# Kernel tuning notes

Measured on AMD Instinct MI355X. Metric: run time of the kernel, lower is better.

The kernel has to match this reference:

```python
import jax, jax.numpy as jnp
import numpy as np

N_HEADS = 32
N_KV = 8
HEAD_DIM = 128
ROPE_THETA = 10000.0
PAST_LEN = 2048


def _rope_cos_sin(position_ids):
    # inv_freq: [head_dim/2]
    inv_freq = 1.0 / (ROPE_THETA ** (jnp.arange(0, HEAD_DIM, 2, dtype=jnp.float32) / HEAD_DIM))
    freqs = position_ids.astype(jnp.float32)[..., None] * inv_freq  # [B, S, hd/2]
    emb = jnp.concatenate([freqs, freqs], axis=-1)  # [B, S, hd]
    return jnp.cos(emb), jnp.sin(emb)


def _rotate_half(x):
    x1, x2 = jnp.split(x, 2, axis=-1)
    return jnp.concatenate([-x2, x1], axis=-1)


def setup_inputs() -> dict:
    key = jax.random.key(0)
    ks = jax.random.split(key, 10)
    B, S = 1, 2048
    IN = 8192
    s = 0.02
    return {
        "hidden_states": jax.random.normal(ks[0], (B, S, IN), jnp.float32),
        "position_ids": (jnp.arange(S, dtype=jnp.int32) + PAST_LEN)[None, :],
        "cache_k": jax.random.normal(ks[1], (B, N_KV, PAST_LEN, HEAD_DIM), jnp.float32),
        "cache_v": jax.random.normal(ks[2], (B, N_KV, PAST_LEN, HEAD_DIM), jnp.float32),
        "Wq": jax.random.normal(ks[3], (N_HEADS * HEAD_DIM, IN), jnp.float32) * s,
        "bq": jax.random.normal(ks[4], (N_HEADS * HEAD_DIM,), jnp.float32) * s,
        "Wk": jax.random.normal(ks[5], (N_KV * HEAD_DIM, IN), jnp.float32) * s,
        "bk": jax.random.normal(ks[6], (N_KV * HEAD_DIM,), jnp.float32) * s,
        "Wv": jax.random.normal(ks[7], (N_KV * HEAD_DIM, IN), jnp.float32) * s,
        "bv": jax.random.normal(ks[8], (N_KV * HEAD_DIM,), jnp.float32) * s,
        "Wo": jax.random.normal(ks[9], (N_HEADS * HEAD_DIM, N_HEADS * HEAD_DIM), jnp.float32) * s,
    }


def reference(hidden_states, position_ids, cache_k, cache_v, Wq, bq, Wk, bk, Wv, bv, Wo):
    B, Sq, _ = hidden_states.shape
    G = N_HEADS // N_KV

    # QKV projections -> [B, H, S, D]
    q = (hidden_states @ Wq.T + bq).reshape(B, Sq, N_HEADS, HEAD_DIM).transpose(0, 2, 1, 3)
    k = (hidden_states @ Wk.T + bk).reshape(B, Sq, N_KV, HEAD_DIM).transpose(0, 2, 1, 3)
    v = (hidden_states @ Wv.T + bv).reshape(B, Sq, N_KV, HEAD_DIM).transpose(0, 2, 1, 3)

    # RoPE
    cos, sin = _rope_cos_sin(position_ids)  # [B, Sq, D]
    cos, sin = cos[:, None], sin[:, None]   # broadcast over heads
    q = q * cos + _rotate_half(q) * sin
    k = k * cos + _rotate_half(k) * sin

    # KV cache concat
    key = jnp.concatenate([cache_k, k], axis=2)   # [B, Kv, Sk, D]
    value = jnp.concatenate([cache_v, v], axis=2)
    Sk = key.shape[2]
    past_len = Sk - Sq

    # GQA attention (grouped einsum == repeat_interleave + SDPA)
    qg = q.reshape(B, N_KV, G, Sq, HEAD_DIM)
    scale = 1.0 / jnp.sqrt(jnp.float32(HEAD_DIM))
    scores = jnp.einsum("bkgqd,bkld->bkgql", qg, key) * scale  # [B, Kv, G, Sq, Sk]

    q_pos = past_len + jnp.arange(Sq)
    mask = jnp.arange(Sk)[None, :] <= q_pos[:, None]  # [Sq, Sk]
    scores = jnp.where(mask[None, None, None], scores, -jnp.inf)
    attn = jax.nn.softmax(scores, axis=-1)

    ctx = jnp.einsum("bkgql,bkld->bkgqd", attn, value)
    ctx = ctx.reshape(B, N_HEADS, Sq, HEAD_DIM).transpose(0, 2, 1, 3).reshape(B, Sq, N_HEADS * HEAD_DIM)
    out = ctx @ Wo.T
    return out, key, value
```

## Files before the change

### kernel.cpp

```cpp
#include <hip/hip_runtime.h>
#include <hip/hip_bf16.h>
#include <math.h>

typedef float f32x4 __attribute__((ext_vector_type(4)));
typedef short s16x8 __attribute__((ext_vector_type(8)));
typedef __bf16 bf16x8 __attribute__((ext_vector_type(8)));

__device__ __forceinline__ unsigned short f2bf(float f) {
  return __builtin_bit_cast(unsigned short, (__bf16)f);
}

__device__ __forceinline__ f32x4 mfma16(s16x8 a, s16x8 b, f32x4 c) {
  return __builtin_amdgcn_mfma_f32_16x16x32_bf16(
      __builtin_bit_cast(bf16x8, a), __builtin_bit_cast(bf16x8, b), c, 0, 0, 0);
}

#define GLDS(gp, lp) __builtin_amdgcn_global_load_lds(                      \
    (__attribute__((address_space(1))) void*)(gp),                          \
    (__attribute__((address_space(3))) void*)(lp), 16, 0, 0)

struct __attribute__((aligned(8))) us4 { unsigned short x, y, z, w; };
__device__ __forceinline__ us4 cvt4(float4 v) {
  us4 r; r.x = f2bf(v.x); r.y = f2bf(v.y); r.z = f2bf(v.z); r.w = f2bf(v.w);
  return r;
}

__global__ __launch_bounds__(256) void conv_all(
    const float4* __restrict__ h, const float4* __restrict__ wq,
    const float4* __restrict__ wk, const float4* __restrict__ wv,
    const float4* __restrict__ wo, const float4* __restrict__ bq,
    const float4* __restrict__ bk, const float4* __restrict__ bv,
    us4* __restrict__ hbf, us4* __restrict__ wqkvbf, us4* __restrict__ wobf,
    float4* __restrict__ biasc)
{
  const unsigned int U = 20973056u;
  const unsigned int stride = gridDim.x * blockDim.x;
  for (unsigned int u = blockIdx.x * blockDim.x + threadIdx.x; u < U; u += stride) {
    if (u < 4194304u) {
      hbf[u] = cvt4(h[u]);
    } else if (u < 12582912u) {
      unsigned int o = u - 4194304u;  wqkvbf[o] = cvt4(wq[o]);
    } else if (u < 14680064u) {
      unsigned int o = u - 12582912u; wqkvbf[8388608u + o] = cvt4(wk[o]);
    } else if (u < 16777216u) {
      unsigned int o = u - 14680064u; wqkvbf[10485760u + o] = cvt4(wv[o]);
    } else if (u < 20971520u) {
      unsigned int o = u - 16777216u; wobf[o] = cvt4(wo[o]);
    } else {
      unsigned int o = u - 20971520u;
      float4 v = (o < 1024u) ? bq[o] : (o < 1280u) ? bk[o - 1024u] : bv[o - 1280u];
      biasc[o] = v;
    }
  }
}

__global__ __launch_bounds__(256) void rope_table(const int* __restrict__ pos_ids,
                                                  float* __restrict__ cost,
                                                  float* __restrict__ sint)
{
  int idx = blockIdx.x * blockDim.x + threadIdx.x;
  if (idx >= 131072) return;
  int s = idx >> 6, i = idx & 63;
  double invf = exp(-((double)i / 64.0) * 9.210340371976184);
  double ang = (double)pos_ids[s] * invf;
  cost[idx] = (float)cos(ang);
  sint[idx] = (float)sin(ang);
}

template<int NF>
__global__ __launch_bounds__(512, 2) void gemm8p(const unsigned short* __restrict__ A,
                                                 const unsigned short* __restrict__ B,
                                                 const float* __restrict__ bias,
                                                 float* __restrict__ C,
                                                 int M, int N, int K)
{
  constexpr int BN = NF * 64;
  constexpr int BUFSZ = 32768 + BN * 128;
  __shared__ char smem[2 * BUFSZ];
  const int tid = threadIdx.x;
  const int l = tid & 63;
  const int w = tid >> 6;
  const int wm = w >> 2, wn = w & 3;
  const int wr = wm * 128;
  const int wc = wn * (16 * NF);
  const int lk16 = (l >> 4) * 16;

  const int nwg = gridDim.x;
  const int s = (blockIdx.x & 7) * (nwg >> 3) + (blockIdx.x >> 3);
  const int NBY = M >> 8;
  const int by = s % NBY, bx = s / NBY;
  const size_t arow0 = (size_t)by * 256;
  const size_t brow0 = (size_t)bx * BN;
  const size_t Kb = (size_t)K * 2;
  const char* Ab = (const char*)A;
  const char* Bb = (const char*)B;

  f32x4 acc[8][NF];
#pragma unroll
  for (int i = 0; i < 8; ++i)
#pragma unroll
    for (int j = 0; j < NF; ++j) acc[i][j] = (f32x4){0.f, 0.f, 0.f, 0.f};

  auto STAGE = [&](int t, char* buf) {
    const size_t k0b = (size_t)t * 128;
#pragma unroll
    for (int cc = 0; cc < 4; ++cc) {
      const int ch = cc * 512 + tid;
      const int r = ch >> 3;
      const int c2s = ((ch & 7) * 16) ^ ((r & 7) << 4);
      GLDS(Ab + (arow0 + r) * Kb + k0b + c2s, buf + ch * 16);
    }
#pragma unroll
    for (int cc = 0; cc < NF; ++cc) {
      const int ch = cc * 512 + tid;
      const int r = ch >> 3;
      const int c2s = ((ch & 7) * 16) ^ ((r & 7) << 4);
      GLDS(Bb + (brow0 + r) * Kb + k0b + c2s, buf + 32768 + ch * 16);
    }
  };

  const int nt = K >> 6;
  STAGE(0, smem);
  asm volatile("s_waitcnt vmcnt(0)" ::: "memory");
  __builtin_amdgcn_s_barrier();

  for (int t = 0; t < nt; ++t) {
    char* cur = smem + (t & 1) * BUFSZ;
    if (t + 1 < nt) STAGE(t + 1, smem + ((t + 1) & 1) * BUFSZ);
    s16x8 bfr[NF][2];
#pragma unroll
    for (int qd = 0; qd < 4; ++qd) {
      s16x8 afr[2][2];
#pragma unroll
      for (int i = 0; i < 2; ++i)
#pragma unroll
        for (int k = 0; k < 2; ++k) {
          const int r = wr + (qd * 2 + i) * 16 + (l & 15);
          const int c2 = k * 64 + lk16;
          afr[i][k] = *(const s16x8*)(cur + (r * 128 + (c2 ^ ((r & 7) << 4))));
        }
      if (qd == 0) {
#pragma unroll
        for (int n = 0; n < NF; ++n)
#pragma unroll
          for (int k = 0; k < 2; ++k) {
            const int r = wc + n * 16 + (l & 15);
            const int c2 = k * 64 + lk16;
            bfr[n][k] = *(const s16x8*)(cur + 32768 + (r * 128 + (c2 ^ ((r & 7) << 4))));
          }
      }
      asm volatile("" ::: "memory");
      __builtin_amdgcn_s_barrier();
      __builtin_amdgcn_s_setprio(1);
#pragma unroll
      for (int i = 0; i < 2; ++i)
#pragma unroll
        for (int n = 0; n < NF; ++n)
#pragma unroll
          for (int k = 0; k < 2; ++k)
            acc[qd * 2 + i][n] = mfma16(afr[i][k], bfr[n][k], acc[qd * 2 + i][n]);
      __builtin_amdgcn_s_setprio(0);
      asm volatile("" ::: "memory");
      __builtin_amdgcn_s_barrier();
    }
    asm volatile("s_waitcnt vmcnt(0)" ::: "memory");
    __builtin_amdgcn_s_barrier();
  }

  const int r0 = (int)arow0 + wr + (l >> 4) * 4;
  const int c0 = (int)brow0 + wc + (l & 15);
#pragma unroll
  for (int mi = 0; mi < 8; ++mi) {
#pragma unroll
    for (int ni = 0; ni < NF; ++ni) {
      const int c = c0 + ni * 16;
      const float bvv = bias ? bias[c] : 0.f;
#pragma unroll
      for (int rr = 0; rr < 4; ++rr) {
        const int r = r0 + mi * 16 + rr;
        C[(size_t)r * N + c] = acc[mi][ni][rr] + bvv;
      }
    }
  }
}

__global__ __launch_bounds__(256) void rope_scatter(
    const float* __restrict__ qkv, const float* __restrict__ cost,
    const float* __restrict__ sint, const float* __restrict__ cache_k,
    const float* __restrict__ cache_v, float* __restrict__ keyout,
    float* __restrict__ valout, unsigned short* __restrict__ qbf,
    char* __restrict__ kswz, char* __restrict__ vswz)
{
  const float rs = 0.08838834764831845f;
  const int stride = gridDim.x * blockDim.x;
  for (int idx = blockIdx.x * blockDim.x + threadIdx.x; idx < 11534336; idx += stride) {
    if (idx < 4194304) {
      int i = idx & 63, hh = (idx >> 6) & 31, s = idx >> 11;
      const float* base = qkv + (size_t)s * 6144 + hh * 128 + i;
      float q1 = base[0], q2 = base[64];
      float c = cost[s * 64 + i], sn = sint[s * 64 + i];
      float o1 = (q1 * c - q2 * sn) * rs, o2 = (q2 * c + q1 * sn) * rs;
      unsigned short* qd = qbf + ((size_t)hh * 2048 + s) * 128 + i;
      qd[0] = f2bf(o1); qd[64] = f2bf(o2);
    } else if (idx < 5242880) {
      int j = idx - 4194304;
      int i = j & 63, kh = (j >> 6) & 7, s = j >> 9;
      const float* base = qkv + (size_t)s * 6144 + 4096 + kh * 128 + i;
      float k1 = base[0], k2 = base[64];
      float c = cost[s * 64 + i], sn = sint[s * 64 + i];
      float o1 = k1 * c - k2 * sn, o2 = k2 * c + k1 * sn;
      float* kd = keyout + ((size_t)kh * 4096 + 2048 + s) * 128 + i;
      kd[0] = o1; kd[64] = o2;
      int t = 32 + (s >> 6), r = s & 63;
      char* tb = kswz + (size_t)(kh * 64 + t) * 16384;
      *(unsigned short*)(tb + ((r * 256 + i * 2) ^ ((r & 7) << 4))) = f2bf(o1);
      *(unsigned short*)(tb + ((r * 256 + (i + 64) * 2) ^ ((r & 7) << 4))) = f2bf(o2);
    } else if (idx < 7340032) {
      int j = idx - 5242880;
      int d = j & 127, kh = (j >> 7) & 7, s = j >> 10;
      float v = qkv[(size_t)s * 6144 + 5120 + kh * 128 + d];
      valout[((size_t)kh * 4096 + 2048 + s) * 128 + d] = v;
      int t = 32 + (s >> 6), c = s & 63;
      char* tb = vswz + (size_t)(kh * 64 + t) * 16384;
      *(unsigned short*)(tb + ((d * 128 + c * 2) ^ ((d & 7) << 4))) = f2bf(v);
    } else if (idx < 9437184) {
      int j = idx - 7340032;
      int d = j & 127, s = (j >> 7) & 2047, kh = j >> 18;
      float v = cache_k[(size_t)(kh * 2048 + s) * 128 + d];
      keyout[((size_t)kh * 4096 + s) * 128 + d] = v;
      int t = s >> 6, r = s & 63;
      char* tb = kswz + (size_t)(kh * 64 + t) * 16384;
      *(unsigned short*)(tb + ((r * 256 + d * 2) ^ ((r & 7) << 4))) = f2bf(v);
    } else {
      int j = idx - 9437184;
      int d = j & 127, s = (j >> 7) & 2047, kh = j >> 18;
      float v = cache_v[(size_t)(kh * 2048 + s) * 128 + d];
      valout[((size_t)kh * 4096 + s) * 128 + d] = v;
      int t = s >> 6, c = s & 63;
      char* tb = vswz + (size_t)(kh * 64 + t) * 16384;
      *(unsigned short*)(tb + ((d * 128 + c * 2) ^ ((d & 7) << 4))) = f2bf(v);
    }
  }
}

__global__ __launch_bounds__(512) void attn_fwd(const unsigned short* __restrict__ qbf,
                                                const char* __restrict__ kswz,
                                                const char* __restrict__ vswz,
                                                unsigned short* __restrict__ ctx)
{
  __shared__ char smem[81920];
  char* Ps = smem + 65536;
  const int tid = threadIdx.x;
  const int l = tid & 63;
  const int w = tid >> 6;
  const int d = blockIdx.x;
  const int b = d >> 5;
  const int qt = (b < 8) ? b : 23 - b;
  const int h = (d & 7) * 4 + ((d >> 3) & 3);
  const int kh = h >> 2;
  const int nt = 2 * qt + 34;
  const int qrow16 = (l >> 4) * 4;
  const float L2E = 1.44269504f;

  s16x8 aq[4];
  {
    const int qr = qt * 128 + w * 16 + (l & 15);
    const unsigned short* qp = qbf + ((size_t)h * 2048 + qr) * 128 + (l >> 4) * 8;
#pragma unroll
    for (int kc = 0; kc < 4; ++kc) aq[kc] = *(const s16x8*)(qp + kc * 32);
  }
  f32x4 o[8];
#pragma unroll
  for (int i = 0; i < 8; ++i) o[i] = (f32x4){0.f, 0.f, 0.f, 0.f};
  float m[4]  = {-1e30f, -1e30f, -1e30f, -1e30f};
  float m2[4] = {-1e30f, -1e30f, -1e30f, -1e30f};
  float ls[4] = {0.f, 0.f, 0.f, 0.f};

  const char* kb0 = kswz + (size_t)kh * (64 * 16384);
  const char* vb0 = vswz + (size_t)kh * (64 * 16384);
  char* Pw = Ps + w * 2048;

  auto STAGE = [&](int t, int c) {
    const char* kb = kb0 + (size_t)t * 16384;
    const char* vb = vb0 + (size_t)t * 16384;
    char* Kt = smem + c * 32768;
    char* Vt = Kt + 16384;
#pragma unroll
    for (int j = 0; j < 2; ++j) {
      const int cw = j * 8 + w;
      GLDS(kb + (cw * 64 + l) * 16, Kt + cw * 1024);
      GLDS(vb + (cw * 64 + l) * 16, Vt + cw * 1024);
    }
  };

  STAGE(0, 0);
  int c = 0;
  for (int t = 0; t < nt; ++t) {
    asm volatile("s_waitcnt vmcnt(0)" ::: "memory");
    __builtin_amdgcn_s_barrier();
    asm volatile("" ::: "memory");
    if (t + 1 < nt) STAGE(t + 1, c ^ 1);
    const char* Kt = smem + c * 32768;
    const char* Vt = Kt + 16384;

    f32x4 s[4];
#pragma unroll
    for (int i = 0; i < 4; ++i) s[i] = (f32x4){0.f, 0.f, 0.f, 0.f};
    __builtin_amdgcn_s_setprio(1);
#pragma unroll
    for (int kc = 0; kc < 4; ++kc) {
      const int d0b = (kc * 32 + (l >> 4) * 8) * 2;
#pragma unroll
      for (int ni = 0; ni < 4; ++ni) {
        const int row = ni * 16 + (l & 15);
        s16x8 kf = *(const s16x8*)(Kt + ((row * 256 + d0b) ^ ((row & 7) << 4)));
        s[ni] = mfma16(aq[kc], kf, s[ni]);
      }
    }
    __builtin_amdgcn_s_setprio(0);
    if (t >= nt - 2) {
      const int qpos_b = 2048 + qt * 128 + w * 16 + qrow16;
      const int kvcol = (l & 15);
#pragma unroll
      for (int ni = 0; ni < 4; ++ni) {
        const int kvpos = t * 64 + ni * 16 + kvcol;
#pragma unroll
        for (int rr = 0; rr < 4; ++rr)
          if (kvpos > qpos_b + rr) s[ni][rr] = -1e30f;
      }
    }
    float rm[4];
#pragma unroll
    for (int rr = 0; rr < 4; ++rr)
      rm[rr] = fmaxf(fmaxf(s[0][rr], s[1][rr]), fmaxf(s[2][rr], s[3][rr]));
#pragma unroll
    for (int rr = 0; rr < 4; ++rr) {
      float v = rm[rr];
      v = fmaxf(v, __shfl_xor(v, 1));
      v = fmaxf(v, __shfl_xor(v, 2));
      v = fmaxf(v, __shfl_xor(v, 4));
      v = fmaxf(v, __shfl_xor(v, 8));
      rm[rr] = v;
    }
    const bool ok = (rm[0] <= m[0] + 8.f) && (rm[1] <= m[1] + 8.f) &&
                    (rm[2] <= m[2] + 8.f) && (rm[3] <= m[3] + 8.f);
    if (!__all(ok)) {
      float fs[4];
#pragma unroll
      for (int rr = 0; rr < 4; ++rr) {
        const float nm = fmaxf(m[rr], rm[rr]);
        fs[rr] = __builtin_amdgcn_exp2f((m[rr] - nm) * L2E);
        m[rr] = nm;
        m2[rr] = nm * L2E;
      }
#pragma unroll
      for (int i = 0; i < 8; ++i)
#pragma unroll
        for (int rr = 0; rr < 4; ++rr) o[i][rr] *= fs[rr];
#pragma unroll
      for (int rr = 0; rr < 4; ++rr) ls[rr] *= fs[rr];
    }
#pragma unroll
    for (int ni = 0; ni < 4; ++ni) {
      const int colb = (ni * 16 + (l & 15)) * 2;
#pragma unroll
      for (int rr = 0; rr < 4; ++rr) {
        const float p = __builtin_amdgcn_exp2f(__builtin_fmaf(s[ni][rr], L2E, -m2[rr]));
        ls[rr] += p;
        const int q = qrow16 + rr;
        *(__bf16*)(Pw + ((q * 128 + colb) ^ ((q & 7) << 4))) = (__bf16)p;
      }
    }
    s16x8 pa[2];
#pragma unroll
    for (int kc2 = 0; kc2 < 2; ++kc2) {
      const int q = l & 15;
      const int kvb = (kc2 * 32 + (l >> 4) * 8) * 2;
      pa[kc2] = *(const s16x8*)(Pw + ((q * 128 + kvb) ^ ((q & 7) << 4)));
    }
    __builtin_amdgcn_s_setprio(1);
#pragma unroll
    for (int sub = 0; sub < 8; ++sub) {
      const int dd = sub * 16 + (l & 15);
#pragma unroll
      for (int kc2 = 0; kc2 < 2; ++kc2) {
        const int kvb = (kc2 * 32 + (l >> 4) * 8) * 2;
        s16x8 vf = *(const s16x8*)(Vt + ((dd * 128 + kvb) ^ ((dd & 7) << 4)));
        o[sub] = mfma16(pa[kc2], vf, o[sub]);
      }
    }
    __builtin_amdgcn_s_setprio(0);
    asm volatile("" ::: "memory");
    c ^= 1;
  }

#pragma unroll
  for (int rr = 0; rr < 4; ++rr) {
    float v = ls[rr];
    v += __shfl_xor(v, 1);
    v += __shfl_xor(v, 2);
    v += __shfl_xor(v, 4);
    v += __shfl_xor(v, 8);
    ls[rr] = 1.0f / v;
  }
  const int r0 = qt * 128 + w * 16 + qrow16;
  const int c0 = h * 128 + (l & 15);
#pragma unroll
  for (int sub = 0; sub < 8; ++sub)
#pragma unroll
    for (int rr = 0; rr < 4; ++rr) {
      const float v = o[sub][rr] * ls[rr];
      ctx[(size_t)(r0 + rr) * 4096 + c0 + sub * 16] = f2bf(v);
    }
}

extern "C" void kernel_launch(void* const* d_in, const int* in_sizes, int n_in,
                              void* d_out, int out_size, void* d_ws, size_t ws_size,
                              hipStream_t stream) {
  (void)in_sizes; (void)n_in; (void)out_size; (void)ws_size;
  const float* hs     = (const float*)d_in[0];
  const int*   pos    = (const int*)d_in[1];
  const float* cachek = (const float*)d_in[2];
  const float* cachev = (const float*)d_in[3];
  const float* Wq     = (const float*)d_in[4];
  const float* bq     = (const float*)d_in[5];
  const float* Wk     = (const float*)d_in[6];
  const float* bk     = (const float*)d_in[7];
  const float* Wv     = (const float*)d_in[8];
  const float* bv     = (const float*)d_in[9];
  const float* Wo     = (const float*)d_in[10];

  float* out    = (float*)d_out;
  float* keyout = out + (size_t)2048 * 4096;
  float* valout = keyout + (size_t)8 * 4096 * 128;

  char* ws = (char*)d_ws;
  unsigned short* hbf    = (unsigned short*)(ws + 0);
  unsigned short* qbf    = (unsigned short*)(ws + 0);
  char*           kswz   = ws + 16777216;
  char*           vswz   = ws + 25165824;
  unsigned short* wqkvbf = (unsigned short*)(ws + 33554432);
  unsigned short* wobf   = (unsigned short*)(ws + 134217728);
  float*          qkvf   = (float*)(ws + 167772160);
  unsigned short* ctxbf  = (unsigned short*)(ws + 167772160);
  float*          cost   = (float*)(ws + 218103808);
  float*          sint   = (float*)(ws + 218628096);
  float*          biasc  = (float*)(ws + 219152384);

  conv_all<<<2048, 256, 0, stream>>>((const float4*)hs, (const float4*)Wq,
                                     (const float4*)Wk, (const float4*)Wv,
                                     (const float4*)Wo, (const float4*)bq,
                                     (const float4*)bk, (const float4*)bv,
                                     (us4*)hbf, (us4*)wqkvbf, (us4*)wobf,
                                     (float4*)biasc);
  rope_table<<<512, 256, 0, stream>>>(pos, cost, sint);
  gemm8p<3><<<256, 512, 0, stream>>>(hbf, wqkvbf, biasc, qkvf, 2048, 6144, 8192);
  rope_scatter<<<2048, 256, 0, stream>>>(qkvf, cost, sint, cachek, cachev,
                                         keyout, valout, qbf, kswz, vswz);
  attn_fwd<<<512, 512, 0, stream>>>(qbf, kswz, vswz, ctxbf);
  gemm8p<2><<<256, 512, 0, stream>>>(ctxbf, wobf, nullptr, out, 2048, 4096, 4096);
}
```

Measured before the change: 637.0 us.

## Process two 16-row query tiles per wave in attention kernel

Attention block now uses 4 waves of 256 threads instead of 8, and each wave handles 32 query rows as two 16-row sub-tiles. Each K and V fragment read from LDS feeds two MFMAs, halving LDS read traffic per unit of compute. The cost is roughly doubled accumulator and score registers per wave, which may lower occupancy or cause spills, and fewer waves are left to hide latency.

```diff
diff --git a/kernel.cpp b/kernel.cpp
--- a/kernel.cpp
+++ b/kernel.cpp
@@ -243,7 +243,7 @@
   }
 }
 
-__global__ __launch_bounds__(512) void attn_fwd(const unsigned short* __restrict__ qbf,
+__global__ __launch_bounds__(256) void attn_fwd(const unsigned short* __restrict__ qbf,
                                                 const char* __restrict__ kswz,
                                                 const char* __restrict__ vswz,
                                                 unsigned short* __restrict__ ctx)
@@ -253,32 +253,38 @@
   const int tid = threadIdx.x;
   const int l = tid & 63;
   const int w = tid >> 6;
+  const int g = l >> 4;
   const int d = blockIdx.x;
   const int b = d >> 5;
   const int qt = (b < 8) ? b : 23 - b;
   const int h = (d & 7) * 4 + ((d >> 3) & 3);
   const int kh = h >> 2;
   const int nt = 2 * qt + 34;
-  const int qrow16 = (l >> 4) * 4;
+  const int qrow16 = g * 4;
   const float L2E = 1.44269504f;
 
-  s16x8 aq[4];
-  {
-    const int qr = qt * 128 + w * 16 + (l & 15);
-    const unsigned short* qp = qbf + ((size_t)h * 2048 + qr) * 128 + (l >> 4) * 8;
-#pragma unroll
-    for (int kc = 0; kc < 4; ++kc) aq[kc] = *(const s16x8*)(qp + kc * 32);
-  }
-  f32x4 o[8];
-#pragma unroll
-  for (int i = 0; i < 8; ++i) o[i] = (f32x4){0.f, 0.f, 0.f, 0.f};
-  float m[4]  = {-1e30f, -1e30f, -1e30f, -1e30f};
-  float m2[4] = {-1e30f, -1e30f, -1e30f, -1e30f};
-  float ls[4] = {0.f, 0.f, 0.f, 0.f};
+  s16x8 aq[2][4];
+#pragma unroll
+  for (int qs = 0; qs < 2; ++qs) {
+    const int qr = qt * 128 + w * 32 + qs * 16 + (l & 15);
+    const unsigned short* qp = qbf + ((size_t)h * 2048 + qr) * 128 + g * 8;
+#pragma unroll
+    for (int kc = 0; kc < 4; ++kc) aq[qs][kc] = *(const s16x8*)(qp + kc * 32);
+  }
+  f32x4 o[2][8];
+#pragma unroll
+  for (int qs = 0; qs < 2; ++qs)
+#pragma unroll
+    for (int i = 0; i < 8; ++i) o[qs][i] = (f32x4){0.f, 0.f, 0.f, 0.f};
+  float m[2][4], m2[2][4], ls[2][4];
+#pragma unroll
+  for (int qs = 0; qs < 2; ++qs)
+#pragma unroll
+    for (int rr = 0; rr < 4; ++rr) { m[qs][rr] = -1e30f; m2[qs][rr] = -1e30f; ls[qs][rr] = 0.f; }
 
   const char* kb0 = kswz + (size_t)kh * (64 * 16384);
   const char* vb0 = vswz + (size_t)kh * (64 * 16384);
-  char* Pw = Ps + w * 2048;
+  char* Pw = Ps + w * 4096;
 
   auto STAGE = [&](int t, int c) {
     const char* kb = kb0 + (size_t)t * 16384;
@@ -286,8 +292,8 @@
     char* Kt = smem + c * 32768;
     char* Vt = Kt + 16384;
 #pragma unroll
-    for (int j = 0; j < 2; ++j) {
-      const int cw = j * 8 + w;
+    for (int j = 0; j < 4; ++j) {
+      const int cw = j * 4 + w;
       GLDS(kb + (cw * 64 + l) * 16, Kt + cw * 1024);
       GLDS(vb + (cw * 64 + l) * 16, Vt + cw * 1024);
     }
@@ -303,90 +309,108 @@
     const char* Kt = smem + c * 32768;
     const char* Vt = Kt + 16384;
 
-    f32x4 s[4];
-#pragma unroll
-    for (int i = 0; i < 4; ++i) s[i] = (f32x4){0.f, 0.f, 0.f, 0.f};
+    f32x4 s[2][4];
+#pragma unroll
+    for (int qs = 0; qs < 2; ++qs)
+#pragma unroll
+      for (int i = 0; i < 4; ++i) s[qs][i] = (f32x4){0.f, 0.f, 0.f, 0.f};
     __builtin_amdgcn_s_setprio(1);
 #pragma unroll
     for (int kc = 0; kc < 4; ++kc) {
-      const int d0b = (kc * 32 + (l >> 4) * 8) * 2;
+      const int d0b = (kc * 32 + g * 8) * 2;
 #pragma unroll
       for (int ni = 0; ni < 4; ++ni) {
         const int row = ni * 16 + (l & 15);
         s16x8 kf = *(const s16x8*)(Kt + ((row * 256 + d0b) ^ ((row & 7) << 4)));
-        s[ni] = mfma16(aq[kc], kf, s[ni]);
+        s[0][ni] = mfma16(aq[0][kc], kf, s[0][ni]);
+        s[1][ni] = mfma16(aq[1][kc], kf, s[1][ni]);
       }
     }
     __builtin_amdgcn_s_setprio(0);
     if (t >= nt - 2) {
-      const int qpos_b = 2048 + qt * 128 + w * 16 + qrow16;
       const int kvcol = (l & 15);
 #pragma unroll
+      for (int qs = 0; qs < 2; ++qs) {
+        const int qpos_b = 2048 + qt * 128 + w * 32 + qs * 16 + qrow16;
+#pragma unroll
+        for (int ni = 0; ni < 4; ++ni) {
+          const int kvpos = t * 64 + ni * 16 + kvcol;
+#pragma unroll
+          for (int rr = 0; rr < 4; ++rr)
+            if (kvpos > qpos_b + rr) s[qs][ni][rr] = -1e30f;
+        }
+      }
+    }
+    float rm[2][4];
+#pragma unroll
+    for (int qs = 0; qs < 2; ++qs)
+#pragma unroll
+      for (int rr = 0; rr < 4; ++rr) {
+        float v = fmaxf(fmaxf(s[qs][0][rr], s[qs][1][rr]),
+                        fmaxf(s[qs][2][rr], s[qs][3][rr]));
+        v = fmaxf(v, __shfl_xor(v, 1));
+        v = fmaxf(v, __shfl_xor(v, 2));
+        v = fmaxf(v, __shfl_xor(v, 4));
+        v = fmaxf(v, __shfl_xor(v, 8));
+        rm[qs][rr] = v;
+      }
+    bool ok = true;
+#pragma unroll
+    for (int qs = 0; qs < 2; ++qs)
+#pragma unroll
+      for (int rr = 0; rr < 4; ++rr) ok = ok && (rm[qs][rr] <= m[qs][rr] + 8.f);
+    if (!__all(ok)) {
+#pragma unroll
+      for (int qs = 0; qs < 2; ++qs) {
+        float fs[4];
+#pragma unroll
+        for (int rr = 0; rr < 4; ++rr) {
+          const float nm = fmaxf(m[qs][rr], rm[qs][rr]);
+          fs[rr] = __builtin_amdgcn_exp2f((m[qs][rr] - nm) * L2E);
+          m[qs][rr] = nm;
+          m2[qs][rr] = nm * L2E;
+        }
+#pragma unroll
+        for (int i = 0; i < 8; ++i)
+#pragma unroll
+          for (int rr = 0; rr < 4; ++rr) o[qs][i][rr] *= fs[rr];
+#pragma unroll
+        for (int rr = 0; rr < 4; ++rr) ls[qs][rr] *= fs[rr];
+      }
+    }
+#pragma unroll
+    for (int qs = 0; qs < 2; ++qs)
+#pragma unroll
       for (int ni = 0; ni < 4; ++ni) {
-        const int kvpos = t * 64 + ni * 16 + kvcol;
-#pragma unroll
-        for (int rr = 0; rr < 4; ++rr)
-          if (kvpos > qpos_b + rr) s[ni][rr] = -1e30f;
-      }
-    }
-    float rm[4];
-#pragma unroll
-    for (int rr = 0; rr < 4; ++rr)
-      rm[rr] = fmaxf(fmaxf(s[0][rr], s[1][rr]), fmaxf(s[2][rr], s[3][rr]));
-#pragma unroll
-    for (int rr = 0; rr < 4; ++rr) {
-      float v = rm[rr];
-      v = fmaxf(v, __shfl_xor(v, 1));
-      v = fmaxf(v, __shfl_xor(v, 2));
-      v = fmaxf(v, __shfl_xor(v, 4));
-      v = fmaxf(v, __shfl_xor(v, 8));
-      rm[rr] = v;
-    }
-    const bool ok = (rm[0] <= m[0] + 8.f) && (rm[1] <= m[1] + 8.f) &&
-                    (rm[2] <= m[2] + 8.f) && (rm[3] <= m[3] + 8.f);
-    if (!__all(ok)) {
-      float fs[4];
-#pragma unroll
-      for (int rr = 0; rr < 4; ++rr) {
-        const float nm = fmaxf(m[rr], rm[rr]);
-        fs[rr] = __builtin_amdgcn_exp2f((m[rr] - nm) * L2E);
-        m[rr] = nm;
-        m2[rr] = nm * L2E;
-      }
-#pragma unroll
-      for (int i = 0; i < 8; ++i)
-#pragma unroll
-        for (int rr = 0; rr < 4; ++rr) o[i][rr] *= fs[rr];
-#pragma unroll
-      for (int rr = 0; rr < 4; ++rr) ls[rr] *= fs[rr];
-    }
-#pragma unroll
-    for (int ni = 0; ni < 4; ++ni) {
-      const int colb = (ni * 16 + (l & 15)) * 2;
-#pragma unroll
-      for (int rr = 0; rr < 4; ++rr) {
-        const float p = __builtin_amdgcn_exp2f(__builtin_fmaf(s[ni][rr], L2E, -m2[rr]));
-        ls[rr] += p;
-        const int q = qrow16 + rr;
-        *(__bf16*)(Pw + ((q * 128 + colb) ^ ((q & 7) << 4))) = (__bf16)p;
-      }
-    }
-    s16x8 pa[2];
-#pragma unroll
-    for (int kc2 = 0; kc2 < 2; ++kc2) {
-      const int q = l & 15;
-      const int kvb = (kc2 * 32 + (l >> 4) * 8) * 2;
-      pa[kc2] = *(const s16x8*)(Pw + ((q * 128 + kvb) ^ ((q & 7) << 4)));
-    }
+        const int colb = (ni * 16 + (l & 15)) * 2;
+#pragma unroll
+        for (int rr = 0; rr < 4; ++rr) {
+          const float p =
+              __builtin_amdgcn_exp2f(__builtin_fmaf(s[qs][ni][rr], L2E, -m2[qs][rr]));
+          ls[qs][rr] += p;
+          const int q = qs * 16 + qrow16 + rr;
+          *(__bf16*)(Pw + ((q * 128 + colb) ^ ((q & 7) << 4))) = (__bf16)p;
+        }
+      }
+    s16x8 pa[2][2];
+#pragma unroll
+    for (int qs = 0; qs < 2; ++qs)
+#pragma unroll
+      for (int kc2 = 0; kc2 < 2; ++kc2) {
+        const int q = qs * 16 + (l & 15);
+        const int kvb = (kc2 * 32 + g * 8) * 2;
+        pa[qs][kc2] = *(const s16x8*)(Pw + ((q * 128 + kvb) ^ ((q & 7) << 4)));
+      }
     __builtin_amdgcn_s_setprio(1);
 #pragma unroll
     for (int sub = 0; sub < 8; ++sub) {
       const int dd = sub * 16 + (l & 15);
 #pragma unroll
       for (int kc2 = 0; kc2 < 2; ++kc2) {
-        const int kvb = (kc2 * 32 + (l >> 4) * 8) * 2;
+        const int kvb = (kc2 * 32 + g * 8) * 2;
         s16x8 vf = *(const s16x8*)(Vt + ((dd * 128 + kvb) ^ ((dd & 7) << 4)));
-        o[sub] = mfma16(pa[kc2], vf, o[sub]);
+        o[0][sub] = mfma16(pa[0][kc2], vf, o[0][sub]);
+        o[1][sub] = mfma16(pa[1][kc2], vf, o[1][sub]);
       }
     }
     __builtin_amdgcn_s_setprio(0);
@@ -395,23 +419,28 @@
   }
 
 #pragma unroll
-  for (int rr = 0; rr < 4; ++rr) {
-    float v = ls[rr];
-    v += __shfl_xor(v, 1);
-    v += __shfl_xor(v, 2);
-    v += __shfl_xor(v, 4);
-    v += __shfl_xor(v, 8);
-    ls[rr] = 1.0f / v;
-  }
-  const int r0 = qt * 128 + w * 16 + qrow16;
+  for (int qs = 0; qs < 2; ++qs)
+#pragma unroll
+    for (int rr = 0; rr < 4; ++rr) {
+      float v = ls[qs][rr];
+      v += __shfl_xor(v, 1);
+      v += __shfl_xor(v, 2);
+      v += __shfl_xor(v, 4);
+      v += __shfl_xor(v, 8);
+      ls[qs][rr] = 1.0f / v;
+    }
   const int c0 = h * 128 + (l & 15);
 #pragma unroll
-  for (int sub = 0; sub < 8; ++sub)
-#pragma unroll
-    for (int rr = 0; rr < 4; ++rr) {
-      const float v = o[sub][rr] * ls[rr];
-      ctx[(size_t)(r0 + rr) * 4096 + c0 + sub * 16] = f2bf(v);
-    }
+  for (int qs = 0; qs < 2; ++qs) {
+    const int r0 = qt * 128 + w * 32 + qs * 16 + qrow16;
+#pragma unroll
+    for (int sub = 0; sub < 8; ++sub)
+#pragma unroll
+      for (int rr = 0; rr < 4; ++rr) {
+        const float v = o[qs][sub][rr] * ls[qs][rr];
+        ctx[(size_t)(r0 + rr) * 4096 + c0 + sub * 16] = f2bf(v);
+      }
+  }
 }
 
 extern "C" void kernel_launch(void* const* d_in, const int* in_sizes, int n_in,
@@ -457,6 +486,6 @@
   gemm8p<3><<<256, 512, 0, stream>>>(hbf, wqkvbf, biasc, qkvf, 2048, 6144, 8192);
   rope_scatter<<<2048, 256, 0, stream>>>(qkvf, cost, sint, cachek, cachev,
                                          keyout, valout, qbf, kswz, vswz);
-  attn_fwd<<<512, 512, 0, stream>>>(qbf, kswz, vswz, ctxbf);
+  attn_fwd<<<512, 256, 0, stream>>>(qbf, kswz, vswz, ctxbf);
   gemm8p<2><<<256, 512, 0, stream>>>(ctxbf, wobf, nullptr, out, 2048, 4096, 4096);
 }
```

Measured after the change: 736.7 us. 1.16x slower.
